# Performance work log

Measured on AMD Instinct MI355X. Metric: run time of the kernel, lower is better.

The kernel has to match this reference:

```python
import jax, jax.numpy as jnp
import numpy as np

N, E, IN, HID, OUT, L = 50000, 800000, 128, 64, 40, 3


def setup_inputs() -> dict:
    key = jax.random.key(0)
    ks = jax.random.split(key, 10)
    x = jax.random.normal(ks[0], (N, IN), jnp.float32)
    edge_index = jax.random.randint(ks[1], (2, E), 0, N, dtype=jnp.int32)

    def u(k, shape, fan_in):
        s = 1.0 / np.sqrt(fan_in)
        return jax.random.uniform(k, shape, jnp.float32, -s, s)

    return {
        "x": x,
        "edge_index": edge_index,
        # former1 (NWGformerF): in -> hidden projection
        "Wf": u(ks[2], (IN, HID), IN),
        "bf": jnp.zeros((HID,), jnp.float32),
        # stacked GCNConv weights (hidden->hidden)
        "conv_W": u(ks[3], (L, HID, HID), HID),
        "conv_b": jnp.zeros((L, HID), jnp.float32),
        # residual linears
        "lin_W": u(ks[4], (L, HID, HID), HID),
        "lin_b": u(ks[5], (L, HID), HID),
        # batchnorm (eval mode: affine with running stats)
        "gamma": jnp.ones((L, HID), jnp.float32),
        "beta": jnp.zeros((L, HID), jnp.float32),
        "run_mean": jnp.zeros((L, HID), jnp.float32),
        "run_var": jnp.ones((L, HID), jnp.float32),
        # output head
        "pred_W": u(ks[6], (HID, OUT), HID),
        "pred_b": jnp.zeros((OUT,), jnp.float32),
    }


def reference(x, edge_index, Wf, bf, conv_W, conv_b, lin_W, lin_b,
              gamma, beta, run_mean, run_var, pred_W, pred_b):
    n = x.shape[0]
    src, dst = edge_index[0], edge_index[1]
    eps = 1e-5

    # GCN symmetric normalization with self-loops: deg over dst (+1 self loop)
    deg = jax.ops.segment_sum(jnp.ones(src.shape[0], x.dtype), dst,
                              num_segments=n) + 1.0
    dinv = jax.lax.rsqrt(deg)                      # [N]
    edge_coef = dinv[src] * dinv[dst]              # [E]
    self_coef = (dinv * dinv)[:, None]             # [N,1]

    def gcn(h, W, b):
        hw = h @ W                                 # [N,HID]
        agg = jax.ops.segment_sum(hw[src] * edge_coef[:, None], dst,
                                  num_segments=n)
        return agg + hw * self_coef + b

    # former1: in -> hidden (dropout is identity in eval mode)
    h = x @ Wf + bf

    for i in range(L):
        h = gcn(h, conv_W[i], conv_b[i]) + h @ lin_W[i] + lin_b[i]  # res
        h = (h - run_mean[i]) * (gamma[i] * jax.lax.rsqrt(run_var[i] + eps)) + beta[i]
        h = jax.nn.relu(h)

    return h @ pred_W + pred_b
```

## Files before the change

### kernel.cpp

```cpp
#include <hip/hip_runtime.h>
#include <hip/hip_bf16.h>
#include <hip/hip_fp16.h>

#define IN_DIM 128
#define HID 64
#define OUT_DIM 40
#define SPAD 68

typedef __hip_bfloat16 bf16;
typedef unsigned short u16;
typedef _Float16 f16;
typedef __attribute__((ext_vector_type(8))) _Float16 f16x8;
typedef __attribute__((ext_vector_type(4))) float f32x4;

__device__ __forceinline__ float b2f(bf16 v) { return __bfloat162float(v); }
__device__ __forceinline__ float relu_f(float x) { return 0.5f * (x + fabsf(x)); }
__device__ __forceinline__ float ldv(const void* p, int i, int is32) {
    return is32 ? ((const float*)p)[i] : b2f(((const bf16*)p)[i]);
}

__global__ void MPNNs_60198261620971_kernel() {}

__global__ void canary_k(float* out, int m) {
    int i = blockIdx.x * blockDim.x + threadIdx.x;
    if (i < m) out[i] = 1234.0f;
}


__global__ void zerodetect_k(unsigned int* __restrict__ c2, int n2,
                             const unsigned int* __restrict__ rv, int* __restrict__ flag) {
    int i = blockIdx.x * blockDim.x + threadIdx.x;
    if (i < n2) c2[i] = 0;
    if (i == 0) flag[0] = (rv[0] == 0x3F800000u) ? 1 : 0;
}

__global__ void count_k(const int* __restrict__ dst, unsigned int* __restrict__ c2,
                        u16* __restrict__ rank, int e, int n) {
    int i = blockIdx.x * blockDim.x + threadIdx.x;
    if (i < e) {
        int d = dst[i];
        u16 r = 0;
        if ((unsigned)d < (unsigned)n) {
            int sh = (d & 1) * 16;
            unsigned old = atomicAdd(&c2[d >> 1], 1u << sh);
            r = (u16)((old >> sh) & 0xFFFFu);
        }
        rank[i] = r;
    }
}

__global__ void scan1_k(const unsigned int* __restrict__ c2, int* __restrict__ row_ptr,
                        int* __restrict__ psum, float* __restrict__ dinv, int n) {
    __shared__ int sdata[1024];
    int i = blockIdx.x * 1024 + threadIdx.x;
    int v = 0;
    if (i < n) v = (int)((c2[i >> 1] >> ((i & 1) * 16)) & 0xFFFFu);
    if (i < n) dinv[i] = rsqrtf((float)v + 1.0f);
    sdata[threadIdx.x] = v;
    __syncthreads();
    for (int off = 1; off < 1024; off <<= 1) {
        int t = (threadIdx.x >= off) ? sdata[threadIdx.x - off] : 0;
        __syncthreads();
        sdata[threadIdx.x] += t;
        __syncthreads();
    }
    if (i < n) row_ptr[i] = sdata[threadIdx.x] - v;
    if (threadIdx.x == 1023) psum[blockIdx.x] = sdata[1023];
}

__global__ void scan2_k(int* __restrict__ psum, int* __restrict__ row_ptr, int nb, int n) {
    __shared__ int sdata[1024];
    int v = (threadIdx.x < nb) ? psum[threadIdx.x] : 0;
    sdata[threadIdx.x] = v;
    __syncthreads();
    for (int off = 1; off < 1024; off <<= 1) {
        int t = (threadIdx.x >= off) ? sdata[threadIdx.x - off] : 0;
        __syncthreads();
        sdata[threadIdx.x] += t;
        __syncthreads();
    }
    if (threadIdx.x < nb) psum[threadIdx.x] = sdata[threadIdx.x] - v;
    if (threadIdx.x == 1023) row_ptr[n] = sdata[1023];
}

__global__ void scan3_k(int* __restrict__ row_ptr, const int* __restrict__ psum, int n) {
    int i = blockIdx.x * blockDim.x + threadIdx.x;
    if (i < n) row_ptr[i] += psum[i >> 10];
}

__global__ void fill_k(const int* __restrict__ src, const int* __restrict__ dst,
                       const int* __restrict__ row_ptr, const u16* __restrict__ rank,
                       u16* __restrict__ col, int e, int n) {
    int i = blockIdx.x * blockDim.x + threadIdx.x;
    if (i < e) {
        int d = dst[i];
        if ((unsigned)d < (unsigned)n)
            col[row_ptr[d] + (int)rank[i]] = (u16)src[i];
    }
}


__global__ __launch_bounds__(256) void former_k(const void* __restrict__ x,
                                                const void* __restrict__ Wf,
                                                const void* __restrict__ bfv,
                                                const int* __restrict__ dflag,
                                                float* __restrict__ h, int n) {
    __shared__ float sW[IN_DIM * HID];
    __shared__ float sx[64 * SPAD];
    int is32 = dflag[0];
    if (is32) {
        const float4* w4 = (const float4*)Wf;
        for (int i = threadIdx.x; i < IN_DIM * HID / 4; i += 256) ((float4*)sW)[i] = w4[i];
    } else {
        for (int i = threadIdx.x; i < IN_DIM * HID; i += 256) sW[i] = b2f(((const bf16*)Wf)[i]);
    }
    int tid = threadIdx.x, cg = tid & 15, rg = tid >> 4;
    int rowBase = blockIdx.x * 64;
    float acc[4][4];
    #pragma unroll
    for (int i = 0; i < 4; i++)
        #pragma unroll
        for (int j = 0; j < 4; j++) acc[i][j] = 0.f;

    for (int p = 0; p < 2; p++) {
        __syncthreads();
        #pragma unroll
        for (int pass = 0; pass < 4; pass++) {
            int r = pass * 16 + (tid >> 4);
            int c = (tid & 15) * 4;
            int gr = rowBase + r;
            float4 v = make_float4(0.f, 0.f, 0.f, 0.f);
            if (gr < n) {
                if (is32) v = *(const float4*)((const float*)x + (size_t)gr * IN_DIM + p * 64 + c);
                else {
                    const bf16* xb = (const bf16*)x + (size_t)gr * IN_DIM + p * 64 + c;
                    v = make_float4(b2f(xb[0]), b2f(xb[1]), b2f(xb[2]), b2f(xb[3]));
                }
            }
            *(float4*)&sx[r * SPAD + c] = v;
        }
        __syncthreads();
        for (int k = 0; k < 64; k += 4) {
            float4 hr[4], w[4];
            #pragma unroll
            for (int i = 0; i < 4; i++) hr[i] = *(float4*)&sx[(rg * 4 + i) * SPAD + k];
            #pragma unroll
            for (int j = 0; j < 4; j++) w[j] = *(float4*)&sW[(p * 64 + k + j) * HID + cg * 4];
            #pragma unroll
            for (int i = 0; i < 4; i++) {
                const float* hh = (const float*)&hr[i];
                #pragma unroll
                for (int j = 0; j < 4; j++) {
                    const float* ww = (const float*)&w[j];
                    acc[i][0] += hh[j] * ww[0];
                    acc[i][1] += hh[j] * ww[1];
                    acc[i][2] += hh[j] * ww[2];
                    acc[i][3] += hh[j] * ww[3];
                }
            }
        }
    }
    float b0 = ldv(bfv, cg * 4 + 0, is32), b1 = ldv(bfv, cg * 4 + 1, is32);
    float b2 = ldv(bfv, cg * 4 + 2, is32), b3 = ldv(bfv, cg * 4 + 3, is32);
    #pragma unroll
    for (int i = 0; i < 4; i++) {
        int r = rowBase + rg * 4 + i;
        if (r < n) {
            float4 o = make_float4(acc[i][0] + b0, acc[i][1] + b1, acc[i][2] + b2, acc[i][3] + b3);
            *(float4*)&h[(size_t)r * HID + cg * 4] = o;
        }
    }
}

__global__ __launch_bounds__(256) void dense_k(float* __restrict__ h,
                                               const void* __restrict__ convW,
                                               const void* __restrict__ linW,
                                               const void* __restrict__ convB,
                                               const void* __restrict__ linB,
                                               const int* __restrict__ dflag,
                                               const float* __restrict__ dinv,
                                               __half* __restrict__ hws, int n, int l) {
    __shared__ __align__(16) f16 wT[2][HID][72];
    int is32 = dflag[0];
    int wOff = l * HID * HID, vOff = l * HID;
    for (int i = threadIdx.x; i < HID * HID; i += 256) {
        int k = i >> 6, nn = i & 63;
        wT[0][nn][k] = (f16)ldv(convW, wOff + i, is32);
        wT[1][nn][k] = (f16)ldv(linW, wOff + i, is32);
    }
    __syncthreads();
    int wave = threadIdx.x >> 6, lane = threadIdx.x & 63;
    int m = lane & 15, quad = lane >> 4;
    int row0 = blockIdx.x * 64 + wave * 16;
    if (row0 >= n) return;
    int ar = row0 + m;
    const float* hp = h + (size_t)((ar < n) ? ar : 0) * HID;
    float4 v0 = *(const float4*)(hp + quad * 8);
    float4 v1 = *(const float4*)(hp + quad * 8 + 4);
    float4 v2 = *(const float4*)(hp + 32 + quad * 8);
    float4 v3 = *(const float4*)(hp + 32 + quad * 8 + 4);
    f16x8 a0 = { (f16)v0.x, (f16)v0.y, (f16)v0.z, (f16)v0.w,
                 (f16)v1.x, (f16)v1.y, (f16)v1.z, (f16)v1.w };
    f16x8 a1 = { (f16)v2.x, (f16)v2.y, (f16)v2.z, (f16)v2.w,
                 (f16)v3.x, (f16)v3.y, (f16)v3.z, (f16)v3.w };
    f32x4 acc[2][4];
    #pragma unroll
    for (int t = 0; t < 2; t++)
        #pragma unroll
        for (int ct = 0; ct < 4; ct++) acc[t][ct] = (f32x4){0.f, 0.f, 0.f, 0.f};
    #pragma unroll
    for (int ct = 0; ct < 4; ct++) {
        int nn = ct * 16 + m;
        f16x8 b00 = *(const f16x8*)&wT[0][nn][quad * 8];
        f16x8 b01 = *(const f16x8*)&wT[0][nn][32 + quad * 8];
        f16x8 b10 = *(const f16x8*)&wT[1][nn][quad * 8];
        f16x8 b11 = *(const f16x8*)&wT[1][nn][32 + quad * 8];
        acc[0][ct] = __builtin_amdgcn_mfma_f32_16x16x32_f16(a0, b00, acc[0][ct], 0, 0, 0);
        acc[0][ct] = __builtin_amdgcn_mfma_f32_16x16x32_f16(a1, b01, acc[0][ct], 0, 0, 0);
        acc[1][ct] = __builtin_amdgcn_mfma_f32_16x16x32_f16(a0, b10, acc[1][ct], 0, 0, 0);
        acc[1][ct] = __builtin_amdgcn_mfma_f32_16x16x32_f16(a1, b11, acc[1][ct], 0, 0, 0);
    }
    float cbv[4];
    #pragma unroll
    for (int ct = 0; ct < 4; ct++)
        cbv[ct] = ldv(convB, vOff + ct * 16 + m, is32) + ldv(linB, vOff + ct * 16 + m, is32);
    #pragma unroll
    for (int r = 0; r < 4; r++) {
        int row = row0 + quad * 4 + r;
        if (row < n) {
            float dv = dinv[row];
            #pragma unroll
            for (int ct = 0; ct < 4; ct++) {
                int colx = ct * 16 + m;
                hws[(size_t)row * HID + colx] = __float2half(acc[0][ct][r] * dv);
                h[(size_t)row * HID + colx] = acc[1][ct][r] + cbv[ct];
            }
        }
    }
}

__global__ __launch_bounds__(256) void agg_k(const __half* __restrict__ hws,
                                             const float* __restrict__ dinv,
                                             const int* __restrict__ row_ptr,
                                             const u16* __restrict__ col,
                                             const void* __restrict__ gamma,
                                             const void* __restrict__ beta,
                                             const void* __restrict__ mean,
                                             const void* __restrict__ var,
                                             const int* __restrict__ dflag,
                                             float* __restrict__ h, int n, int l) {
    int gwave = (blockIdx.x * blockDim.x + threadIdx.x) >> 6;
    int lane = threadIdx.x & 63;
    int nw = (gridDim.x * blockDim.x) >> 6;
    int is32 = dflag[0];
    int vOff = l * HID;
    float mn = ldv(mean, vOff + lane, is32);
    float sc = ldv(gamma, vOff + lane, is32) * rsqrtf(ldv(var, vOff + lane, is32) + 1e-5f);
    float bt = ldv(beta, vOff + lane, is32);
    for (int v = gwave; v < n; v += nw) {
        int s0 = row_ptr[v], s1 = row_ptr[v + 1];
        float a0 = __half2float(hws[(size_t)v * HID + lane]);
        float a1 = 0.f, a2 = 0.f, a3 = 0.f, a4 = 0.f, a5 = 0.f, a6 = 0.f, a7 = 0.f;
        for (int j0 = s0; j0 < s1; j0 += 64) {
            int myidx = (j0 + lane < s1) ? (int)col[j0 + lane] : 0;
            int cnt = min(64, s1 - j0);
            int t = 0;
            for (; t + 8 <= cnt; t += 8) {
                int i0 = __shfl(myidx, t);
                int i1 = __shfl(myidx, t + 1);
                int i2 = __shfl(myidx, t + 2);
                int i3 = __shfl(myidx, t + 3);
                int i4 = __shfl(myidx, t + 4);
                int i5 = __shfl(myidx, t + 5);
                int i6 = __shfl(myidx, t + 6);
                int i7 = __shfl(myidx, t + 7);
                i0 = ((unsigned)i0 < (unsigned)n) ? i0 : 0;
                i1 = ((unsigned)i1 < (unsigned)n) ? i1 : 0;
                i2 = ((unsigned)i2 < (unsigned)n) ? i2 : 0;
                i3 = ((unsigned)i3 < (unsigned)n) ? i3 : 0;
                i4 = ((unsigned)i4 < (unsigned)n) ? i4 : 0;
                i5 = ((unsigned)i5 < (unsigned)n) ? i5 : 0;
                i6 = ((unsigned)i6 < (unsigned)n) ? i6 : 0;
                i7 = ((unsigned)i7 < (unsigned)n) ? i7 : 0;
                __half g0 = hws[(size_t)i0 * HID + lane];
                __half g1 = hws[(size_t)i1 * HID + lane];
                __half g2 = hws[(size_t)i2 * HID + lane];
                __half g3 = hws[(size_t)i3 * HID + lane];
                __half g4 = hws[(size_t)i4 * HID + lane];
                __half g5 = hws[(size_t)i5 * HID + lane];
                __half g6 = hws[(size_t)i6 * HID + lane];
                __half g7 = hws[(size_t)i7 * HID + lane];
                a0 += __half2float(g0); a1 += __half2float(g1);
                a2 += __half2float(g2); a3 += __half2float(g3);
                a4 += __half2float(g4); a5 += __half2float(g5);
                a6 += __half2float(g6); a7 += __half2float(g7);
            }
            for (; t < cnt; t++) {
                int s = __shfl(myidx, t);
                s = ((unsigned)s < (unsigned)n) ? s : 0;
                a0 += __half2float(hws[(size_t)s * HID + lane]);
            }
        }
        float acc = ((a0 + a1) + (a2 + a3)) + ((a4 + a5) + (a6 + a7));
        float val = dinv[v] * acc + h[(size_t)v * HID + lane];
        val = (val - mn) * sc + bt;
        h[(size_t)v * HID + lane] = relu_f(val);
    }
}

__global__ __launch_bounds__(256) void pred_k(const float* __restrict__ h,
                                              const void* __restrict__ pW,
                                              const void* __restrict__ pb,
                                              const int* __restrict__ dflag,
                                              void* __restrict__ out, int n) {
    __shared__ float sW[HID * OUT_DIM];
    __shared__ float sh[64 * SPAD];
    int is32 = dflag[0];
    if (is32) {
        const float4* w4 = (const float4*)pW;
        for (int i = threadIdx.x; i < HID * OUT_DIM / 4; i += 256) ((float4*)sW)[i] = w4[i];
    } else {
        for (int i = threadIdx.x; i < HID * OUT_DIM; i += 256) sW[i] = b2f(((const bf16*)pW)[i]);
    }
    int tid = threadIdx.x, cg = tid & 15, rg = tid >> 4;
    int rowBase = blockIdx.x * 64;
    #pragma unroll
    for (int pass = 0; pass < 4; pass++) {
        int r = pass * 16 + (tid >> 4);
        int c = (tid & 15) * 4;
        int gr = rowBase + r;
        float4 v = (gr < n) ? *(const float4*)&h[(size_t)gr * HID + c] : make_float4(0.f, 0.f, 0.f, 0.f);
        *(float4*)&sh[r * SPAD + c] = v;
    }
    __syncthreads();
    if (cg < 10) {
        float acc[4][4];
        #pragma unroll
        for (int i = 0; i < 4; i++)
            #pragma unroll
            for (int j = 0; j < 4; j++) acc[i][j] = 0.f;
        for (int k = 0; k < 64; k += 4) {
            float4 hr[4], w[4];
            #pragma unroll
            for (int i = 0; i < 4; i++) hr[i] = *(float4*)&sh[(rg * 4 + i) * SPAD + k];
            #pragma unroll
            for (int j = 0; j < 4; j++) w[j] = *(float4*)&sW[(k + j) * OUT_DIM + cg * 4];
            #pragma unroll
            for (int i = 0; i < 4; i++) {
                const float* hh = (const float*)&hr[i];
                #pragma unroll
                for (int j = 0; j < 4; j++) {
                    const float* ww = (const float*)&w[j];
                    acc[i][0] += hh[j] * ww[0];
                    acc[i][1] += hh[j] * ww[1];
                    acc[i][2] += hh[j] * ww[2];
                    acc[i][3] += hh[j] * ww[3];
                }
            }
        }
        float b0 = ldv(pb, cg * 4 + 0, is32), b1 = ldv(pb, cg * 4 + 1, is32);
        float b2 = ldv(pb, cg * 4 + 2, is32), b3 = ldv(pb, cg * 4 + 3, is32);
        #pragma unroll
        for (int i = 0; i < 4; i++) {
            int r = rowBase + rg * 4 + i;
            if (r < n) {
                if (is32) {
                    float4 o = make_float4(acc[i][0] + b0, acc[i][1] + b1, acc[i][2] + b2, acc[i][3] + b3);
                    *(float4*)((float*)out + (size_t)r * OUT_DIM + cg * 4) = o;
                } else {
                    bf16* ob = (bf16*)out + (size_t)r * OUT_DIM + cg * 4;
                    ob[0] = __float2bfloat16(acc[i][0] + b0);
                    ob[1] = __float2bfloat16(acc[i][1] + b1);
                    ob[2] = __float2bfloat16(acc[i][2] + b2);
                    ob[3] = __float2bfloat16(acc[i][3] + b3);
                }
            }
        }
    }
}


extern "C" void kernel_launch(void* const* d_in, const int* in_sizes, int n_in,
                              void* d_out, int out_size, void* d_ws, size_t ws_size,
                              hipStream_t stream) {
    const void* x     = d_in[0];
    const int*  ei    = (const int*)d_in[1];
    const void* Wf    = d_in[2];
    const void* bfv   = d_in[3];
    const void* convW = d_in[4];
    const void* convB = d_in[5];
    const void* linW  = d_in[6];
    const void* linB  = d_in[7];
    const void* gamma = d_in[8];
    const void* beta  = d_in[9];
    const void* rmean = d_in[10];
    const void* rvar  = d_in[11];
    const void* pW    = d_in[12];
    const void* pb    = d_in[13];

    const int n = in_sizes[0] / IN_DIM;
    const int e = in_sizes[1] / 2;
    const int L = in_sizes[5] / HID;
    const int n2 = (n + 1) / 2;

    const int* src = ei;
    const int* dst = ei + e;

    char* ws = (char*)d_ws;
    size_t off = 0;
    auto take = [&](size_t bytes) {
        char* p = ws + off;
        off = (off + bytes + 255) & ~(size_t)255;
        return p;
    };
    float*        h       = (float*)take((size_t)n * HID * 4);
    __half*       hws     = (__half*)take((size_t)n * HID * 2);
    float*        dinv    = (float*)take((size_t)n * 4);
    unsigned int* c2      = (unsigned int*)take((size_t)n2 * 4);
    int*          row_ptr = (int*)take((size_t)(n + 1) * 4);
    u16*          rank    = (u16*)take((size_t)e * 2);
    u16*          colbuf  = (u16*)take((size_t)e * 2);
    int*          psum    = (int*)take(1024 * 4);
    int*          dflag   = (int*)take(256);

    if (off > ws_size || n > 65535) {
        canary_k<<<(out_size + 255) / 256, 256, 0, stream>>>((float*)d_out, out_size);
        return;
    }

    const int eblocks = (e + 255) / 256;
    const int nblocks = (n + 255) / 256;
    const int nb1024  = (n + 1023) / 1024;
    const int nb64    = (n + 63) / 64;

    zerodetect_k<<<(n2 + 255) / 256, 256, 0, stream>>>(c2, n2, (const unsigned int*)rvar, dflag);
    count_k<<<eblocks, 256, 0, stream>>>(dst, c2, rank, e, n);
    scan1_k<<<nb1024, 1024, 0, stream>>>(c2, row_ptr, psum, dinv, n);
    scan2_k<<<1, 1024, 0, stream>>>(psum, row_ptr, nb1024, n);
    scan3_k<<<nblocks, 256, 0, stream>>>(row_ptr, psum, n);
    fill_k<<<eblocks, 256, 0, stream>>>(src, dst, row_ptr, rank, colbuf, e, n);

    former_k<<<nb64, 256, 0, stream>>>(x, Wf, bfv, dflag, h, n);

    for (int l = 0; l < L; l++) {
        dense_k<<<nb64, 256, 0, stream>>>(h, convW, linW, convB, linB,
                                          dflag, dinv, hws, n, l);
        agg_k<<<2048, 256, 0, stream>>>(hws, dinv, row_ptr, colbuf,
                                        gamma, beta, rmean, rvar, dflag, h, n, l);
    }

    pred_k<<<nb64, 256, 0, stream>>>(h, pW, pb, dflag, (void*)d_out, n);
}
```

Baseline: 328.0 us.

## Replicate degree counters per XCC and gather two edges per wave in aggregation

Degree counting now keeps one atomic counter array per XCC, selected by reading the hardware XCC id register, so atomics stay local to each die. Per-replica prefix offsets are computed in the scan and then used when filling the CSR. The aggregation kernel has each half-wave load half2 pairs from a different neighbour, so one wave processes two edges per gather step. The two halves are then combined with a shuffle. This adds extra zeroing and base-offset buffers, and it limits per-replica rank to 13 bits.

Measured after the change: 325.7 us. About the same (-0.7%).

```diff
diff --git a/kernel.cpp b/kernel.cpp
--- a/kernel.cpp
+++ b/kernel.cpp
@@ -27,35 +27,52 @@
 }
 
 
-__global__ void zerodetect_k(unsigned int* __restrict__ c2, int n2,
+__global__ void zerodetect_k(unsigned int* __restrict__ c2r, int nw,
                              const unsigned int* __restrict__ rv, int* __restrict__ flag) {
     int i = blockIdx.x * blockDim.x + threadIdx.x;
-    if (i < n2) c2[i] = 0;
+    if (i < nw) c2r[i] = 0;
     if (i == 0) flag[0] = (rv[0] == 0x3F800000u) ? 1 : 0;
 }
 
-__global__ void count_k(const int* __restrict__ dst, unsigned int* __restrict__ c2,
-                        u16* __restrict__ rank, int e, int n) {
+__global__ void count_k(const int* __restrict__ dst, unsigned int* __restrict__ c2r,
+                        u16* __restrict__ rank, int e, int n, int n2) {
     int i = blockIdx.x * blockDim.x + threadIdx.x;
-    if (i < e) {
-        int d = dst[i];
-        u16 r = 0;
-        if ((unsigned)d < (unsigned)n) {
-            int sh = (d & 1) * 16;
-            unsigned old = atomicAdd(&c2[d >> 1], 1u << sh);
-            r = (u16)((old >> sh) & 0xFFFFu);
-        }
-        rank[i] = r;
-    }
-}
-
-__global__ void scan1_k(const unsigned int* __restrict__ c2, int* __restrict__ row_ptr,
-                        int* __restrict__ psum, float* __restrict__ dinv, int n) {
+    if (i >= e) return;
+    int xcc = __builtin_amdgcn_s_getreg((31u << 11) | 20) & 7;
+    int d = dst[i];
+    u16 r = 0;
+    if ((unsigned)d < (unsigned)n) {
+        int sh = (d & 1) * 16;
+        unsigned old = atomicAdd(&c2r[(size_t)xcc * n2 + (d >> 1)], 1u << sh);
+        r = (u16)(((old >> sh) & 0x1FFFu) | ((unsigned)xcc << 13));
+    }
+    rank[i] = r;
+}
+
+__global__ void scan1_k(const unsigned int* __restrict__ c2r, int* __restrict__ row_ptr,
+                        int* __restrict__ psum, float* __restrict__ dinv,
+                        u16* __restrict__ base, int n, int n2) {
     __shared__ int sdata[1024];
     int i = blockIdx.x * 1024 + threadIdx.x;
     int v = 0;
-    if (i < n) v = (int)((c2[i >> 1] >> ((i & 1) * 16)) & 0xFFFFu);
-    if (i < n) dinv[i] = rsqrtf((float)v + 1.0f);
+    if (i < n) {
+        int sh = (i & 1) * 16;
+        int acc = 0;
+        u16 b[8];
+        #pragma unroll
+        for (int r = 0; r < 8; r++) {
+            b[r] = (u16)acc;
+            acc += (int)((c2r[(size_t)r * n2 + (i >> 1)] >> sh) & 0xFFFFu);
+        }
+        v = acc;
+        uint4 bw;
+        bw.x = (unsigned)b[0] | ((unsigned)b[1] << 16);
+        bw.y = (unsigned)b[2] | ((unsigned)b[3] << 16);
+        bw.z = (unsigned)b[4] | ((unsigned)b[5] << 16);
+        bw.w = (unsigned)b[6] | ((unsigned)b[7] << 16);
+        *(uint4*)&base[(size_t)i * 8] = bw;
+        dinv[i] = rsqrtf((float)v + 1.0f);
+    }
     sdata[threadIdx.x] = v;
     __syncthreads();
     for (int off = 1; off < 1024; off <<= 1) {
@@ -90,12 +107,15 @@
 
 __global__ void fill_k(const int* __restrict__ src, const int* __restrict__ dst,
                        const int* __restrict__ row_ptr, const u16* __restrict__ rank,
-                       u16* __restrict__ col, int e, int n) {
+                       const u16* __restrict__ base, u16* __restrict__ col, int e, int n) {
     int i = blockIdx.x * blockDim.x + threadIdx.x;
     if (i < e) {
         int d = dst[i];
-        if ((unsigned)d < (unsigned)n)
-            col[row_ptr[d] + (int)rank[i]] = (u16)src[i];
+        if ((unsigned)d < (unsigned)n) {
+            u16 rw = rank[i];
+            int rep = rw >> 13, lr = rw & 0x1FFF;
+            col[row_ptr[d] + (int)base[(size_t)d * 8 + rep] + lr] = (u16)src[i];
+        }
     }
 }
 
@@ -252,59 +272,59 @@
     int gwave = (blockIdx.x * blockDim.x + threadIdx.x) >> 6;
     int lane = threadIdx.x & 63;
     int nw = (gridDim.x * blockDim.x) >> 6;
+    int half = lane >> 5, c = lane & 31;
+    const __half2* hws2 = (const __half2*)hws;
     int is32 = dflag[0];
     int vOff = l * HID;
-    float mn = ldv(mean, vOff + lane, is32);
-    float sc = ldv(gamma, vOff + lane, is32) * rsqrtf(ldv(var, vOff + lane, is32) + 1e-5f);
-    float bt = ldv(beta, vOff + lane, is32);
+    float mn0 = ldv(mean, vOff + 2 * c, is32),     mn1 = ldv(mean, vOff + 2 * c + 1, is32);
+    float sc0 = ldv(gamma, vOff + 2 * c, is32) * rsqrtf(ldv(var, vOff + 2 * c, is32) + 1e-5f);
+    float sc1 = ldv(gamma, vOff + 2 * c + 1, is32) * rsqrtf(ldv(var, vOff + 2 * c + 1, is32) + 1e-5f);
+    float bt0 = ldv(beta, vOff + 2 * c, is32),     bt1 = ldv(beta, vOff + 2 * c + 1, is32);
     for (int v = gwave; v < n; v += nw) {
         int s0 = row_ptr[v], s1 = row_ptr[v + 1];
-        float a0 = __half2float(hws[(size_t)v * HID + lane]);
-        float a1 = 0.f, a2 = 0.f, a3 = 0.f, a4 = 0.f, a5 = 0.f, a6 = 0.f, a7 = 0.f;
+        float2 a[8];
+        #pragma unroll
+        for (int g = 0; g < 8; g++) a[g] = make_float2(0.f, 0.f);
+        if (half == 0) {
+            float2 s = __half22float2(hws2[(size_t)v * 32 + c]);
+            a[0].x += s.x; a[0].y += s.y;
+        }
         for (int j0 = s0; j0 < s1; j0 += 64) {
             int myidx = (j0 + lane < s1) ? (int)col[j0 + lane] : 0;
             int cnt = min(64, s1 - j0);
             int t = 0;
-            for (; t + 8 <= cnt; t += 8) {
-                int i0 = __shfl(myidx, t);
-                int i1 = __shfl(myidx, t + 1);
-                int i2 = __shfl(myidx, t + 2);
-                int i3 = __shfl(myidx, t + 3);
-                int i4 = __shfl(myidx, t + 4);
-                int i5 = __shfl(myidx, t + 5);
-                int i6 = __shfl(myidx, t + 6);
-                int i7 = __shfl(myidx, t + 7);
-                i0 = ((unsigned)i0 < (unsigned)n) ? i0 : 0;
-                i1 = ((unsigned)i1 < (unsigned)n) ? i1 : 0;
-                i2 = ((unsigned)i2 < (unsigned)n) ? i2 : 0;
-                i3 = ((unsigned)i3 < (unsigned)n) ? i3 : 0;
-                i4 = ((unsigned)i4 < (unsigned)n) ? i4 : 0;
-                i5 = ((unsigned)i5 < (unsigned)n) ? i5 : 0;
-                i6 = ((unsigned)i6 < (unsigned)n) ? i6 : 0;
-                i7 = ((unsigned)i7 < (unsigned)n) ? i7 : 0;
-                __half g0 = hws[(size_t)i0 * HID + lane];
-                __half g1 = hws[(size_t)i1 * HID + lane];
-                __half g2 = hws[(size_t)i2 * HID + lane];
-                __half g3 = hws[(size_t)i3 * HID + lane];
-                __half g4 = hws[(size_t)i4 * HID + lane];
-                __half g5 = hws[(size_t)i5 * HID + lane];
-                __half g6 = hws[(size_t)i6 * HID + lane];
-                __half g7 = hws[(size_t)i7 * HID + lane];
-                a0 += __half2float(g0); a1 += __half2float(g1);
-                a2 += __half2float(g2); a3 += __half2float(g3);
-                a4 += __half2float(g4); a5 += __half2float(g5);
-                a6 += __half2float(g6); a7 += __half2float(g7);
-            }
-            for (; t < cnt; t++) {
-                int s = __shfl(myidx, t);
-                s = ((unsigned)s < (unsigned)n) ? s : 0;
-                a0 += __half2float(hws[(size_t)s * HID + lane]);
-            }
-        }
-        float acc = ((a0 + a1) + (a2 + a3)) + ((a4 + a5) + (a6 + a7));
-        float val = dinv[v] * acc + h[(size_t)v * HID + lane];
-        val = (val - mn) * sc + bt;
-        h[(size_t)v * HID + lane] = relu_f(val);
+            for (; t + 16 <= cnt; t += 16) {
+                #pragma unroll
+                for (int g = 0; g < 8; g++) {
+                    int idx = __shfl(myidx, t + 2 * g + half);
+                    idx = ((unsigned)idx < (unsigned)n) ? idx : 0;
+                    float2 p = __half22float2(hws2[(size_t)idx * 32 + c]);
+                    a[g].x += p.x; a[g].y += p.y;
+                }
+            }
+            for (; t < cnt; t += 2) {
+                int has = (t + half) < cnt;
+                int sel = t + half; if (sel >= cnt) sel = cnt - 1;
+                int idx = __shfl(myidx, sel);
+                idx = ((unsigned)idx < (unsigned)n) ? idx : 0;
+                float2 p = __half22float2(hws2[(size_t)idx * 32 + c]);
+                if (has) { a[0].x += p.x; a[0].y += p.y; }
+            }
+        }
+        float ax = ((a[0].x + a[1].x) + (a[2].x + a[3].x)) + ((a[4].x + a[5].x) + (a[6].x + a[7].x));
+        float ay = ((a[0].y + a[1].y) + (a[2].y + a[3].y)) + ((a[4].y + a[5].y) + (a[6].y + a[7].y));
+        float px = __shfl(ax, c + 32);
+        float py = __shfl(ay, c + 32);
+        if (half == 0) {
+            float dv = dinv[v];
+            float2 basev = *(const float2*)&h[(size_t)v * HID + 2 * c];
+            float vx = dv * (ax + px) + basev.x;
+            float vy = dv * (ay + py) + basev.y;
+            vx = (vx - mn0) * sc0 + bt0;
+            vy = (vy - mn1) * sc1 + bt1;
+            float2 o = make_float2(relu_f(vx), relu_f(vy));
+            *(float2*)&h[(size_t)v * HID + 2 * c] = o;
+        }
     }
 }
 
@@ -416,7 +436,8 @@
     float*        h       = (float*)take((size_t)n * HID * 4);
     __half*       hws     = (__half*)take((size_t)n * HID * 2);
     float*        dinv    = (float*)take((size_t)n * 4);
-    unsigned int* c2      = (unsigned int*)take((size_t)n2 * 4);
+    unsigned int* c2r     = (unsigned int*)take((size_t)8 * n2 * 4);
+    u16*          base    = (u16*)take((size_t)n * 8 * 2);
     int*          row_ptr = (int*)take((size_t)(n + 1) * 4);
     u16*          rank    = (u16*)take((size_t)e * 2);
     u16*          colbuf  = (u16*)take((size_t)e * 2);
@@ -432,13 +453,15 @@
     const int nblocks = (n + 255) / 256;
     const int nb1024  = (n + 1023) / 1024;
     const int nb64    = (n + 63) / 64;
-
-    zerodetect_k<<<(n2 + 255) / 256, 256, 0, stream>>>(c2, n2, (const unsigned int*)rvar, dflag);
-    count_k<<<eblocks, 256, 0, stream>>>(dst, c2, rank, e, n);
-    scan1_k<<<nb1024, 1024, 0, stream>>>(c2, row_ptr, psum, dinv, n);
+    const int nwords  = 8 * n2;
+
+    zerodetect_k<<<(nwords + 255) / 256, 256, 0, stream>>>(c2r, nwords,
+                                                           (const unsigned int*)rvar, dflag);
+    count_k<<<eblocks, 256, 0, stream>>>(dst, c2r, rank, e, n, n2);
+    scan1_k<<<nb1024, 1024, 0, stream>>>(c2r, row_ptr, psum, dinv, base, n, n2);
     scan2_k<<<1, 1024, 0, stream>>>(psum, row_ptr, nb1024, n);
     scan3_k<<<nblocks, 256, 0, stream>>>(row_ptr, psum, n);
-    fill_k<<<eblocks, 256, 0, stream>>>(src, dst, row_ptr, rank, colbuf, e, n);
+    fill_k<<<eblocks, 256, 0, stream>>>(src, dst, row_ptr, rank, base, colbuf, e, n);
 
     former_k<<<nb64, 256, 0, stream>>>(x, Wf, bfv, dflag, h, n);
 
```
